# Optimization experiments

Measured on AMD Instinct MI355X. Metric: run time of the kernel, lower is better.

The kernel has to match this reference:

```python
import jax, jax.numpy as jnp
import numpy as np

B, L, D = 16, 1024, 256  # batch, c_len == q_len (required by the expand/add in the source), 2*d_model


def mask_logits(x, m):
    # Faithful to the source's (unusual) masking: x*m + x*(1-m)*1e30
    return x * m + x * (1.0 - m) * 1e30


def setup_inputs() -> dict:
    key = jax.random.key(0)
    k = jax.random.split(key, 7)
    c = jax.random.normal(k[0], (B, L, D), dtype=jnp.float32)
    q = jax.random.normal(k[1], (B, L, D), dtype=jnp.float32)
    c_mask = jnp.ones((B, 1, L), dtype=jnp.float32)
    q_mask = jnp.ones((B, 1, L), dtype=jnp.float32)
    # Learned parameters (nn.Parameter zeros in the source; random here so the test is non-degenerate)
    c_weight = jax.random.normal(k[2], (D, 1), dtype=jnp.float32) * 0.05
    q_weight = jax.random.normal(k[3], (D, 1), dtype=jnp.float32) * 0.05
    cq_weight = jax.random.normal(k[4], (1, 1, D), dtype=jnp.float32) * 0.05
    bias = jnp.zeros((1,), dtype=jnp.float32)
    return {"c": c, "q": q, "c_mask": c_mask, "q_mask": q_mask,
            "c_weight": c_weight, "q_weight": q_weight,
            "cq_weight": cq_weight, "bias": bias}


def reference(c, q, c_mask, q_mask, c_weight, q_weight, cq_weight, bias):
    # Dropout treated as identity (inference) for a deterministic reference.
    s0 = jnp.matmul(c, c_weight)                      # [B, L, 1] -> broadcasts over q_len
    s1 = jnp.swapaxes(jnp.matmul(c, q_weight), 1, 2)  # [B, 1, L] (source uses c here, not q)
    s2 = jnp.einsum('bid,bjd->bij', c * cq_weight, q) # [B, L, L]
    S = s0 + s1 + s2 + bias                           # trilinear similarity
    S1 = jax.nn.softmax(mask_logits(S, q_mask), axis=-1)              # [B, Lc, Lq]
    C2Q = jnp.matmul(S1, q)                                           # [B, Lc, D]
    # torch F.softmax with no dim on a 3D tensor defaults to dim=0 (legacy behavior) -> axis=0
    S2 = jax.nn.softmax(mask_logits(jnp.swapaxes(S, 1, 2), c_mask), axis=0)  # [B, Lq, Lc]
    S2 = jnp.matmul(S1, S2)                                           # [B, Lc, Lc]
    Q2C = jnp.matmul(S2, c)                                           # [B, Lc, D]
    # torch.cat default dim=0 -> [4B, Lc, D]
    return jnp.concatenate((c, C2Q, c * C2Q, c * Q2C), axis=0)
```

## Files before the change

kernel.cpp:

```cpp
#include <hip/hip_runtime.h>

typedef __bf16 bf16;
typedef _Float16 f16;
typedef __attribute__((ext_vector_type(8))) __bf16 bf16x8;
typedef __attribute__((ext_vector_type(4))) __bf16 bf16x4;
typedef __attribute__((ext_vector_type(8))) _Float16 f16x8;
typedef __attribute__((ext_vector_type(4))) _Float16 f16x4;
typedef __attribute__((ext_vector_type(4))) float f32x4;

constexpr int Bn = 16, Ln = 1024, Dn = 256;

__device__ __forceinline__ float maskf(float m) { return m + (1.0f - m) * 1e30f; }

__device__ __forceinline__ void gload16(const void* g, void* l) {
  __builtin_amdgcn_global_load_lds((const __attribute__((address_space(1))) void*)g,
                                   (__attribute__((address_space(3))) void*)l, 16, 0, 0);
}

#define VMCNT(N) asm volatile("s_waitcnt vmcnt(" #N ")" ::: "memory")
#define LGKM0 asm volatile("s_waitcnt lgkmcnt(0)" ::: "memory")
#define BARR                                  \
  do {                                        \
    asm volatile("" ::: "memory");            \
    __builtin_amdgcn_s_barrier();             \
    asm volatile("" ::: "memory");            \
  } while (0)

__device__ __forceinline__ void stageB128(const bf16* __restrict__ B, int ldb, int k0,
                                          bf16* lB, int tid, int wid) {
#pragma unroll
  for (int p = 0; p < 2; ++p) {
    int c0 = tid + (p << 8);
    int row = c0 >> 2, kk = (c0 & 3) << 3;
    gload16(B + (size_t)row * ldb + k0 + kk, lB + ((p << 8) + (wid << 6)) * 8);
  }
}

__device__ __forceinline__ void stage512(const bf16* __restrict__ G, int ldg, int k0,
                                         bf16* L, int tid, int wid) {
#pragma unroll
  for (int p = 0; p < 2; ++p) {
    int u = tid + (p << 9);
    int row = u >> 3, s = u & 7;
    int kk = ((s ^ (row & 7)) << 3);
    gload16(G + (size_t)row * ldg + k0 + kk, L + ((p << 9) + (wid << 6)) * 8);
  }
}

__device__ __forceinline__ const bf16* swzp(const bf16* L, int row, int slot) {
  return L + row * 64 + ((slot ^ (row & 7)) << 3);
}

__global__ __launch_bounds__(256) void k_prep2(
    const float* __restrict__ c, const float* __restrict__ q,
    const float* __restrict__ cw, const float* __restrict__ qw,
    const float* __restrict__ cqw, bf16* __restrict__ cm, bf16* __restrict__ qb,
    bf16* __restrict__ cT, bf16* __restrict__ qT,
    float* __restrict__ s0, float* __restrict__ s1, float* __restrict__ outc) {
  __shared__ __align__(16) bf16 tc[32][264];
  __shared__ __align__(16) bf16 tq[32][264];
  int blk = blockIdx.x;
  int b = blk >> 5;
  int l0 = (blk & 31) << 5;
  int t = threadIdx.x;
  int rl = t >> 3;
  int c0 = (t & 7) << 5;
  int grow = b * Ln + l0 + rl;
  size_t base = (size_t)grow * Dn + c0;
  float4 cv[8], qv[8];
#pragma unroll
  for (int k = 0; k < 8; ++k) {
    cv[k] = *(const float4*)&c[base + k * 4];
    qv[k] = *(const float4*)&q[base + k * 4];
  }
  float d0 = 0.f, d1 = 0.f;
#pragma unroll
  for (int k = 0; k < 8; ++k) {
    float4 w = *(const float4*)&cw[c0 + k * 4];
    float4 u = *(const float4*)&qw[c0 + k * 4];
    d0 += cv[k].x * w.x + cv[k].y * w.y + cv[k].z * w.z + cv[k].w * w.w;
    d1 += cv[k].x * u.x + cv[k].y * u.y + cv[k].z * u.z + cv[k].w * u.w;
  }
  d0 += __shfl_xor(d0, 1); d0 += __shfl_xor(d0, 2); d0 += __shfl_xor(d0, 4);
  d1 += __shfl_xor(d1, 1); d1 += __shfl_xor(d1, 2); d1 += __shfl_xor(d1, 4);
  if ((t & 7) == 0) { s0[grow] = d0; s1[grow] = d1; }
#pragma unroll
  for (int k = 0; k < 8; ++k) *(float4*)&outc[base + k * 4] = cv[k];
#pragma unroll
  for (int k2 = 0; k2 < 4; ++k2) {
    float4 m0 = *(const float4*)&cqw[c0 + k2 * 8];
    float4 m1 = *(const float4*)&cqw[c0 + k2 * 8 + 4];
    bf16x8 vm, vq, vc;
#pragma unroll
    for (int e = 0; e < 8; ++e) {
      float cvv = ((const float*)&cv[k2 * 2 + (e >> 2)])[e & 3];
      float qvv = ((const float*)&qv[k2 * 2 + (e >> 2)])[e & 3];
      float mw = (e < 4) ? ((const float*)&m0)[e] : ((const float*)&m1)[e - 4];
      vm[e] = (bf16)(cvv * mw);
      vq[e] = (bf16)qvv;
      vc[e] = (bf16)cvv;
    }
    *(bf16x8*)&cm[base + k2 * 8] = vm;
    *(bf16x8*)&qb[base + k2 * 8] = vq;
    *(bf16x8*)&tc[rl][c0 + k2 * 8] = vc;
    *(bf16x8*)&tq[rl][c0 + k2 * 8] = vq;
  }
  __syncthreads();
  int d = t;
  size_t tb = ((size_t)b * Dn + d) * Ln + l0;
  bf16x8 o[4];
#pragma unroll
  for (int j = 0; j < 4; ++j)
#pragma unroll
    for (int e = 0; e < 8; ++e) o[j][e] = tc[j * 8 + e][d];
#pragma unroll
  for (int j = 0; j < 4; ++j) *(bf16x8*)&cT[tb + j * 8] = o[j];
#pragma unroll
  for (int j = 0; j < 4; ++j)
#pragma unroll
    for (int e = 0; e < 8; ++e) o[j][e] = tq[j * 8 + e][d];
#pragma unroll
  for (int j = 0; j < 4; ++j) *(bf16x8*)&qT[tb + j * 8] = o[j];
}

__global__ __launch_bounds__(256) void g_s(const bf16* __restrict__ Am,
                                           const bf16* __restrict__ Bm,
                                           const float* __restrict__ s0,
                                           const float* __restrict__ s1,
                                           const float* __restrict__ bias,
                                           f16* __restrict__ S) {
  __shared__ __align__(16) bf16 lds[2][256 * 32];
  int f = blockIdx.x;
  int o = (f & 7) * 128 + (f >> 3);
  int bx = o & 7, by = (o >> 3) & 7, b = o >> 6;
  const bf16* Ab = Am + (size_t)b * Ln * Dn + (size_t)by * 128 * Dn;
  const bf16* Bb = Bm + (size_t)b * Ln * Dn + (size_t)bx * 128 * Dn;
  const int tid = threadIdx.x, wid = tid >> 6, lane = tid & 63;
  const int r = lane & 15, h = lane >> 4, wr = wid >> 1, wc = wid & 1;
  f32x4 acc[4][4];
  f32x4 zero = {0.f, 0.f, 0.f, 0.f};
#pragma unroll
  for (int i = 0; i < 4; ++i)
#pragma unroll
    for (int j = 0; j < 4; ++j) acc[i][j] = zero;

  stageB128(Ab, Dn, 0, &lds[0][0], tid, wid);
  stageB128(Bb, Dn, 0, &lds[0][128 * 32], tid, wid);
  for (int t = 0; t < 8; ++t) {
    int cur = t & 1;
    if (t < 7) {
      stageB128(Ab, Dn, (t + 1) * 32, &lds[cur ^ 1][0], tid, wid);
      stageB128(Bb, Dn, (t + 1) * 32, &lds[cur ^ 1][128 * 32], tid, wid);
      VMCNT(4);
    } else {
      VMCNT(0);
    }
    BARR;
    const bf16* lA = &lds[cur][0];
    const bf16* lB = &lds[cur][128 * 32];
    bf16x8 av[4], bv[4];
#pragma unroll
    for (int i = 0; i < 4; ++i) {
      av[i] = *(const bf16x8*)(lA + ((wr << 6) + (i << 4) + r) * 32 + (h << 3));
      bv[i] = *(const bf16x8*)(lB + ((wc << 6) + (i << 4) + r) * 32 + (h << 3));
    }
#pragma unroll
    for (int i = 0; i < 4; ++i)
#pragma unroll
      for (int j = 0; j < 4; ++j)
        acc[i][j] = __builtin_amdgcn_mfma_f32_16x16x32_bf16(av[i], bv[j], acc[i][j], 0, 0, 0);
    LGKM0; BARR;
  }
  int grow = by * 128 + wr * 64, gcol = bx * 128 + wc * 64;
  float bvv = bias[0];
  size_t sb = (size_t)b * Ln * Ln;
#pragma unroll
  for (int j = 0; j < 4; ++j) {
    int n = gcol + j * 16 + r;
    float v1 = s1[b * Ln + n];
#pragma unroll
    for (int i = 0; i < 4; ++i) {
      int mb = grow + i * 16 + h * 4;
#pragma unroll
      for (int g = 0; g < 4; ++g) {
        float v0 = s0[b * Ln + mb + g];
        S[sb + (size_t)(mb + g) * Ln + n] = (f16)(acc[i][j][g] + v0 + v1 + bvv);
      }
    }
  }
}

__global__ __launch_bounds__(256) void k_rowsoftmax(const f16* __restrict__ S,
                                                    const float* __restrict__ qmask,
                                                    bf16* __restrict__ P1) {
  int t = threadIdx.x;
  int row = blockIdx.x * 4 + (t >> 6);
  int b = row >> 10;
  int lane = t & 63;
  const f16* Sr = S + (size_t)row * Ln;
  const float* qm = qmask + (size_t)b * Ln;
  float v[16];
  float mx = -3.4e38f;
#pragma unroll
  for (int p = 0; p < 2; ++p) {
    f16x8 x = ((const f16x8*)Sr)[lane + (p << 6)];
    float4 m0 = ((const float4*)qm)[(lane + (p << 6)) * 2];
    float4 m1 = ((const float4*)qm)[(lane + (p << 6)) * 2 + 1];
    float mm[8] = {m0.x, m0.y, m0.z, m0.w, m1.x, m1.y, m1.z, m1.w};
#pragma unroll
    for (int e = 0; e < 8; ++e) {
      float xv = (float)x[e] * maskf(mm[e]);
      v[8 * p + e] = xv;
      mx = fmaxf(mx, xv);
    }
  }
#pragma unroll
  for (int off = 32; off; off >>= 1) mx = fmaxf(mx, __shfl_xor(mx, off));
  float sum = 0.f;
#pragma unroll
  for (int k = 0; k < 16; ++k) {
    v[k] = __expf(v[k] - mx);
    sum += v[k];
  }
#pragma unroll
  for (int off = 32; off; off >>= 1) sum += __shfl_xor(sum, off);
  float inv = 1.0f / sum;
  bf16* Pr = P1 + (size_t)row * Ln;
#pragma unroll
  for (int p = 0; p < 2; ++p) {
    bf16x8 o;
#pragma unroll
    for (int e = 0; e < 8; ++e) o[e] = (bf16)(v[8 * p + e] * inv);
    ((bf16x8*)Pr)[lane + (p << 6)] = o;
  }
}

__global__ __launch_bounds__(256) void k_bp2(const f16* __restrict__ S,
                                             const float* __restrict__ cmask,
                                             bf16* __restrict__ P2) {
  __shared__ __align__(16) bf16 tile[16][32][36];
  int i0 = blockIdx.y * 32, j0 = blockIdx.x * 32;
  int t = threadIdx.x;
  int ti = t >> 3, tj4 = (t & 7) << 2;
  int i = i0 + ti;
  const f16* Sp = S + (size_t)i * Ln + j0 + tj4;
  float fm[16];
#pragma unroll
  for (int b = 0; b < 16; ++b) fm[b] = maskf(cmask[b * Ln + i]);
  f16x4 u[16];
#pragma unroll
  for (int b = 0; b < 16; ++b) u[b] = *(const f16x4*)(Sp + (size_t)b * Ln * Ln);
  float m[4] = {-3.4e38f, -3.4e38f, -3.4e38f, -3.4e38f};
#pragma unroll
  for (int b = 0; b < 16; ++b)
#pragma unroll
    for (int g = 0; g < 4; ++g) m[g] = fmaxf(m[g], (float)u[b][g] * fm[b]);
  float e[16][4];
  float s[4] = {0.f, 0.f, 0.f, 0.f};
#pragma unroll
  for (int b = 0; b < 16; ++b)
#pragma unroll
    for (int g = 0; g < 4; ++g) {
      e[b][g] = __expf((float)u[b][g] * fm[b] - m[g]);
      s[g] += e[b][g];
    }
#pragma unroll
  for (int g = 0; g < 4; ++g) s[g] = 1.0f / s[g];
#pragma unroll
  for (int b = 0; b < 16; ++b)
#pragma unroll
    for (int g = 0; g < 4; ++g) tile[b][tj4 + g][ti] = (bf16)(e[b][g] * s[g]);
  __syncthreads();
  int jl = t >> 3, i4 = (t & 7) << 2;
#pragma unroll
  for (int b = 0; b < 16; ++b) {
    *(bf16x4*)&P2[((size_t)b * Ln + j0 + jl) * Ln + i0 + i4] =
        *(const bf16x4*)&tile[b][jl][i4];
  }
}

__global__ __launch_bounds__(512) void g_t(const bf16* __restrict__ cT,
                                           const bf16* __restrict__ P2,
                                           bf16* __restrict__ TT) {
  __shared__ __align__(16) bf16 lds[2][2 * 128 * 64];
  int f = blockIdx.x;
  int o = (f & 7) * 32 + (f >> 3);
  int b = o >> 4, md = (o >> 3) & 1, nb = o & 7;
  const bf16* Ab = cT + (size_t)b * Dn * Ln + (size_t)md * 128 * Ln;
  const bf16* Bb = P2 + (size_t)b * Ln * Ln + (size_t)nb * 128 * Ln;
  const int tid = threadIdx.x, wid = tid >> 6, lane = tid & 63;
  const int r = lane & 15, h = lane >> 4, wr = wid >> 2, wc = wid & 3;
  f32x4 acc[4][2];
  f32x4 zero = {0.f, 0.f, 0.f, 0.f};
#pragma unroll
  for (int i = 0; i < 4; ++i)
#pragma unroll
    for (int j = 0; j < 2; ++j) acc[i][j] = zero;

  stage512(Ab, Ln, 0, &lds[0][0], tid, wid);
  stage512(Bb, Ln, 0, &lds[0][8192], tid, wid);
  for (int t = 0; t < 16; ++t) {
    int cur = t & 1;
    if (t < 15) {
      stage512(Ab, Ln, (t + 1) * 64, &lds[cur ^ 1][0], tid, wid);
      stage512(Bb, Ln, (t + 1) * 64, &lds[cur ^ 1][8192], tid, wid);
      VMCNT(4);
    } else {
      VMCNT(0);
    }
    BARR;
    const bf16* lA = &lds[cur][0];
    const bf16* lB = &lds[cur][8192];
#pragma unroll
    for (int kk2 = 0; kk2 < 2; ++kk2) {
      int slot = (kk2 << 2) | h;
      bf16x8 av[4], bv[2];
#pragma unroll
      for (int i = 0; i < 4; ++i)
        av[i] = *(const bf16x8*)swzp(lA, (wr << 6) + (i << 4) + r, slot);
#pragma unroll
      for (int j = 0; j < 2; ++j)
        bv[j] = *(const bf16x8*)swzp(lB, (wc << 5) + (j << 4) + r, slot);
#pragma unroll
      for (int i = 0; i < 4; ++i)
#pragma unroll
        for (int j = 0; j < 2; ++j)
          acc[i][j] = __builtin_amdgcn_mfma_f32_16x16x32_bf16(av[i], bv[j], acc[i][j], 0, 0, 0);
    }
    LGKM0; BARR;
  }
  size_t ob = (size_t)b * Dn * Ln;
  int dbase = md * 128 + wr * 64, cbase = nb * 128 + wc * 32;
#pragma unroll
  for (int i = 0; i < 4; ++i)
#pragma unroll
    for (int j = 0; j < 2; ++j) {
      int n = cbase + j * 16 + r;
#pragma unroll
      for (int g = 0; g < 4; ++g)
        TT[ob + (size_t)(dbase + i * 16 + h * 4 + g) * Ln + n] = (bf16)acc[i][j][g];
    }
}

__global__ __launch_bounds__(512) void g_cq(const bf16* __restrict__ P1,
                                            const bf16* __restrict__ qT,
                                            const bf16* __restrict__ TT,
                                            const float* __restrict__ c,
                                            float* __restrict__ out) {
  __shared__ __align__(16) bf16 lds[2][3 * 128 * 64];
  int f = blockIdx.x;
  int o = (f & 7) * 32 + (f >> 3);
  int b = o >> 4, by = (o >> 1) & 7, bx = o & 1;
  const bf16* Ab = P1 + (size_t)b * Ln * Ln + (size_t)by * 128 * Ln;
  const bf16* B1 = qT + (size_t)b * Dn * Ln + (size_t)bx * 128 * Ln;
  const bf16* B2 = TT + (size_t)b * Dn * Ln + (size_t)bx * 128 * Ln;
  const int tid = threadIdx.x, wid = tid >> 6, lane = tid & 63;
  const int r = lane & 15, h = lane >> 4, wr = wid >> 2, wc = wid & 3;
  f32x4 acc1[4][2], acc2[4][2];
  f32x4 zero = {0.f, 0.f, 0.f, 0.f};
#pragma unroll
  for (int i = 0; i < 4; ++i)
#pragma unroll
    for (int j = 0; j < 2; ++j) { acc1[i][j] = zero; acc2[i][j] = zero; }

  stage512(Ab, Ln, 0, &lds[0][0], tid, wid);
  stage512(B1, Ln, 0, &lds[0][8192], tid, wid);
  stage512(B2, Ln, 0, &lds[0][16384], tid, wid);
  for (int t = 0; t < 16; ++t) {
    int cur = t & 1;
    if (t < 15) {
      stage512(Ab, Ln, (t + 1) * 64, &lds[cur ^ 1][0], tid, wid);
      stage512(B1, Ln, (t + 1) * 64, &lds[cur ^ 1][8192], tid, wid);
      stage512(B2, Ln, (t + 1) * 64, &lds[cur ^ 1][16384], tid, wid);
      VMCNT(6);
    } else {
      VMCNT(0);
    }
    BARR;
    const bf16* lA = &lds[cur][0];
    const bf16* lB1 = &lds[cur][8192];
    const bf16* lB2 = &lds[cur][16384];
#pragma unroll
    for (int kk2 = 0; kk2 < 2; ++kk2) {
      int slot = (kk2 << 2) | h;
      bf16x8 av[4], bv[2];
#pragma unroll
      for (int i = 0; i < 4; ++i)
        av[i] = *(const bf16x8*)swzp(lA, (wr << 6) + (i << 4) + r, slot);
#pragma unroll
      for (int j = 0; j < 2; ++j)
        bv[j] = *(const bf16x8*)swzp(lB1, (wc << 5) + (j << 4) + r, slot);
#pragma unroll
      for (int i = 0; i < 4; ++i)
#pragma unroll
        for (int j = 0; j < 2; ++j)
          acc1[i][j] = __builtin_amdgcn_mfma_f32_16x16x32_bf16(av[i], bv[j], acc1[i][j], 0, 0, 0);
#pragma unroll
      for (int j = 0; j < 2; ++j)
        bv[j] = *(const bf16x8*)swzp(lB2, (wc << 5) + (j << 4) + r, slot);
#pragma unroll
      for (int i = 0; i < 4; ++i)
#pragma unroll
        for (int j = 0; j < 2; ++j)
          acc2[i][j] = __builtin_amdgcn_mfma_f32_16x16x32_bf16(av[i], bv[j], acc2[i][j], 0, 0, 0);
    }
    LGKM0; BARR;
  }

  int grow = by * 128 + wr * 64, gcol = bx * 128 + wc * 32;
  const float* cb = c + (size_t)b * Ln * Dn;
  float* o1 = out + (size_t)(1 * Bn + b) * Ln * Dn;
  float* o2 = out + (size_t)(2 * Bn + b) * Ln * Dn;
  float* o3 = out + (size_t)(3 * Bn + b) * Ln * Dn;
#pragma unroll
  for (int j = 0; j < 2; ++j) {
    int n = gcol + j * 16 + r;
#pragma unroll
    for (int i = 0; i < 4; ++i) {
      int mb = grow + i * 16 + h * 4;
#pragma unroll
      for (int g = 0; g < 4; ++g) {
        float v1 = acc1[i][j][g];
        float v2 = acc2[i][j][g];
        size_t off = (size_t)(mb + g) * Dn + n;
        float cc = cb[off];
        o1[off] = v1;
        o2[off] = cc * v1;
        o3[off] = cc * v2;
      }
    }
  }
}

extern "C" void kernel_launch(void* const* d_in, const int* in_sizes, int n_in,
                              void* d_out, int out_size, void* d_ws, size_t ws_size,
                              hipStream_t stream) {
  const float* c = (const float*)d_in[0];
  const float* q = (const float*)d_in[1];
  const float* cmask = (const float*)d_in[2];
  const float* qmask = (const float*)d_in[3];
  const float* cw = (const float*)d_in[4];
  const float* qw = (const float*)d_in[5];
  const float* cqw = (const float*)d_in[6];
  const float* bias = (const float*)d_in[7];
  float* out = (float*)d_out;

  char* w = (char*)d_ws;
  f16* S = (f16*)w;       w += (size_t)Bn * Ln * Ln * 2;
  bf16* P1 = (bf16*)w;    w += (size_t)Bn * Ln * Ln * 2;
  bf16* P2 = (bf16*)w;    w += (size_t)Bn * Ln * Ln * 2;
  bf16* cm = (bf16*)w;    w += (size_t)Bn * Ln * Dn * 2;
  bf16* qb = (bf16*)w;    w += (size_t)Bn * Ln * Dn * 2;
  bf16* cT = (bf16*)w;    w += (size_t)Bn * Dn * Ln * 2;
  bf16* qT = (bf16*)w;    w += (size_t)Bn * Dn * Ln * 2;
  bf16* TT = (bf16*)w;    w += (size_t)Bn * Dn * Ln * 2;
  float* s0 = (float*)w;  w += (size_t)Bn * Ln * 4;
  float* s1 = (float*)w;  w += (size_t)Bn * Ln * 4;
  if ((size_t)(w - (char*)d_ws) > ws_size) return;

  k_prep2<<<dim3(Bn * Ln / 32), 256, 0, stream>>>(c, q, cw, qw, cqw, cm, qb, cT, qT, s0, s1, out);
  g_s<<<dim3(1024), 256, 0, stream>>>(cm, qb, s0, s1, bias, S);
  k_rowsoftmax<<<dim3(Bn * Ln / 4), 256, 0, stream>>>(S, qmask, P1);
  k_bp2<<<dim3(Ln / 32, Ln / 32), 256, 0, stream>>>(S, cmask, P2);
  g_t<<<dim3(256), 512, 0, stream>>>(cT, P2, TT);
  g_cq<<<dim3(256), 512, 0, stream>>>(P1, qT, TT, c, out);
}
```

Measured before the change: 117.6 us.

## Retile S GEMM to 512 threads with swizzled K64 stages; merge softmax kernels

```diff
diff --git a/kernel.cpp b/kernel.cpp
--- a/kernel.cpp
+++ b/kernel.cpp
@@ -25,16 +25,6 @@
     __builtin_amdgcn_s_barrier();             \
     asm volatile("" ::: "memory");            \
   } while (0)
-
-__device__ __forceinline__ void stageB128(const bf16* __restrict__ B, int ldb, int k0,
-                                          bf16* lB, int tid, int wid) {
-#pragma unroll
-  for (int p = 0; p < 2; ++p) {
-    int c0 = tid + (p << 8);
-    int row = c0 >> 2, kk = (c0 & 3) << 3;
-    gload16(B + (size_t)row * ldb + k0 + kk, lB + ((p << 8) + (wid << 6)) * 8);
-  }
-}
 
 __device__ __forceinline__ void stage512(const bf16* __restrict__ G, int ldg, int k0,
                                          bf16* L, int tid, int wid) {
@@ -123,59 +113,64 @@
   for (int j = 0; j < 4; ++j) *(bf16x8*)&qT[tb + j * 8] = o[j];
 }
 
-__global__ __launch_bounds__(256) void g_s(const bf16* __restrict__ Am,
+__global__ __launch_bounds__(512) void g_s(const bf16* __restrict__ Am,
                                            const bf16* __restrict__ Bm,
                                            const float* __restrict__ s0,
                                            const float* __restrict__ s1,
                                            const float* __restrict__ bias,
                                            f16* __restrict__ S) {
-  __shared__ __align__(16) bf16 lds[2][256 * 32];
+  __shared__ __align__(16) bf16 lds[2][2 * 128 * 64];
   int f = blockIdx.x;
   int o = (f & 7) * 128 + (f >> 3);
   int bx = o & 7, by = (o >> 3) & 7, b = o >> 6;
   const bf16* Ab = Am + (size_t)b * Ln * Dn + (size_t)by * 128 * Dn;
   const bf16* Bb = Bm + (size_t)b * Ln * Dn + (size_t)bx * 128 * Dn;
   const int tid = threadIdx.x, wid = tid >> 6, lane = tid & 63;
-  const int r = lane & 15, h = lane >> 4, wr = wid >> 1, wc = wid & 1;
-  f32x4 acc[4][4];
+  const int r = lane & 15, h = lane >> 4, wr = wid >> 2, wc = wid & 3;
+  f32x4 acc[4][2];
   f32x4 zero = {0.f, 0.f, 0.f, 0.f};
 #pragma unroll
   for (int i = 0; i < 4; ++i)
 #pragma unroll
-    for (int j = 0; j < 4; ++j) acc[i][j] = zero;
-
-  stageB128(Ab, Dn, 0, &lds[0][0], tid, wid);
-  stageB128(Bb, Dn, 0, &lds[0][128 * 32], tid, wid);
-  for (int t = 0; t < 8; ++t) {
+    for (int j = 0; j < 2; ++j) acc[i][j] = zero;
+
+  stage512(Ab, Dn, 0, &lds[0][0], tid, wid);
+  stage512(Bb, Dn, 0, &lds[0][8192], tid, wid);
+  for (int t = 0; t < 4; ++t) {
     int cur = t & 1;
-    if (t < 7) {
-      stageB128(Ab, Dn, (t + 1) * 32, &lds[cur ^ 1][0], tid, wid);
-      stageB128(Bb, Dn, (t + 1) * 32, &lds[cur ^ 1][128 * 32], tid, wid);
+    if (t < 3) {
+      stage512(Ab, Dn, (t + 1) * 64, &lds[cur ^ 1][0], tid, wid);
+      stage512(Bb, Dn, (t + 1) * 64, &lds[cur ^ 1][8192], tid, wid);
       VMCNT(4);
     } else {
       VMCNT(0);
     }
     BARR;
     const bf16* lA = &lds[cur][0];
-    const bf16* lB = &lds[cur][128 * 32];
-    bf16x8 av[4], bv[4];
-#pragma unroll
-    for (int i = 0; i < 4; ++i) {
-      av[i] = *(const bf16x8*)(lA + ((wr << 6) + (i << 4) + r) * 32 + (h << 3));
-      bv[i] = *(const bf16x8*)(lB + ((wc << 6) + (i << 4) + r) * 32 + (h << 3));
-    }
-#pragma unroll
-    for (int i = 0; i < 4; ++i)
-#pragma unroll
-      for (int j = 0; j < 4; ++j)
-        acc[i][j] = __builtin_amdgcn_mfma_f32_16x16x32_bf16(av[i], bv[j], acc[i][j], 0, 0, 0);
+    const bf16* lB = &lds[cur][8192];
+#pragma unroll
+    for (int kk2 = 0; kk2 < 2; ++kk2) {
+      int slot = (kk2 << 2) | h;
+      bf16x8 av[4], bv[2];
+#pragma unroll
+      for (int i = 0; i < 4; ++i)
+        av[i] = *(const bf16x8*)swzp(lA, (wr << 6) + (i << 4) + r, slot);
+#pragma unroll
+      for (int j = 0; j < 2; ++j)
+        bv[j] = *(const bf16x8*)swzp(lB, (wc << 5) + (j << 4) + r, slot);
+#pragma unroll
+      for (int i = 0; i < 4; ++i)
+#pragma unroll
+        for (int j = 0; j < 2; ++j)
+          acc[i][j] = __builtin_amdgcn_mfma_f32_16x16x32_bf16(av[i], bv[j], acc[i][j], 0, 0, 0);
+    }
     LGKM0; BARR;
   }
-  int grow = by * 128 + wr * 64, gcol = bx * 128 + wc * 64;
+  int grow = by * 128 + wr * 64, gcol = bx * 128 + wc * 32;
   float bvv = bias[0];
   size_t sb = (size_t)b * Ln * Ln;
 #pragma unroll
-  for (int j = 0; j < 4; ++j) {
+  for (int j = 0; j < 2; ++j) {
     int n = gcol + j * 16 + r;
     float v1 = s1[b * Ln + n];
 #pragma unroll
@@ -190,92 +185,92 @@
   }
 }
 
-__global__ __launch_bounds__(256) void k_rowsoftmax(const f16* __restrict__ S,
-                                                    const float* __restrict__ qmask,
-                                                    bf16* __restrict__ P1) {
+__global__ __launch_bounds__(256) void k_sm(const f16* __restrict__ S,
+                                            const float* __restrict__ qmask,
+                                            const float* __restrict__ cmask,
+                                            bf16* __restrict__ P1,
+                                            bf16* __restrict__ P2) {
+  __shared__ __align__(16) bf16 tile[16][32][36];
+  int blk = blockIdx.x;
   int t = threadIdx.x;
-  int row = blockIdx.x * 4 + (t >> 6);
-  int b = row >> 10;
-  int lane = t & 63;
-  const f16* Sr = S + (size_t)row * Ln;
-  const float* qm = qmask + (size_t)b * Ln;
-  float v[16];
-  float mx = -3.4e38f;
-#pragma unroll
-  for (int p = 0; p < 2; ++p) {
-    f16x8 x = ((const f16x8*)Sr)[lane + (p << 6)];
-    float4 m0 = ((const float4*)qm)[(lane + (p << 6)) * 2];
-    float4 m1 = ((const float4*)qm)[(lane + (p << 6)) * 2 + 1];
-    float mm[8] = {m0.x, m0.y, m0.z, m0.w, m1.x, m1.y, m1.z, m1.w};
-#pragma unroll
-    for (int e = 0; e < 8; ++e) {
-      float xv = (float)x[e] * maskf(mm[e]);
-      v[8 * p + e] = xv;
-      mx = fmaxf(mx, xv);
-    }
-  }
-#pragma unroll
-  for (int off = 32; off; off >>= 1) mx = fmaxf(mx, __shfl_xor(mx, off));
-  float sum = 0.f;
-#pragma unroll
-  for (int k = 0; k < 16; ++k) {
-    v[k] = __expf(v[k] - mx);
-    sum += v[k];
-  }
-#pragma unroll
-  for (int off = 32; off; off >>= 1) sum += __shfl_xor(sum, off);
-  float inv = 1.0f / sum;
-  bf16* Pr = P1 + (size_t)row * Ln;
-#pragma unroll
-  for (int p = 0; p < 2; ++p) {
-    bf16x8 o;
-#pragma unroll
-    for (int e = 0; e < 8; ++e) o[e] = (bf16)(v[8 * p + e] * inv);
-    ((bf16x8*)Pr)[lane + (p << 6)] = o;
-  }
-}
-
-__global__ __launch_bounds__(256) void k_bp2(const f16* __restrict__ S,
-                                             const float* __restrict__ cmask,
-                                             bf16* __restrict__ P2) {
-  __shared__ __align__(16) bf16 tile[16][32][36];
-  int i0 = blockIdx.y * 32, j0 = blockIdx.x * 32;
-  int t = threadIdx.x;
-  int ti = t >> 3, tj4 = (t & 7) << 2;
-  int i = i0 + ti;
-  const f16* Sp = S + (size_t)i * Ln + j0 + tj4;
-  float fm[16];
-#pragma unroll
-  for (int b = 0; b < 16; ++b) fm[b] = maskf(cmask[b * Ln + i]);
-  f16x4 u[16];
-#pragma unroll
-  for (int b = 0; b < 16; ++b) u[b] = *(const f16x4*)(Sp + (size_t)b * Ln * Ln);
-  float m[4] = {-3.4e38f, -3.4e38f, -3.4e38f, -3.4e38f};
-#pragma unroll
-  for (int b = 0; b < 16; ++b)
-#pragma unroll
-    for (int g = 0; g < 4; ++g) m[g] = fmaxf(m[g], (float)u[b][g] * fm[b]);
-  float e[16][4];
-  float s[4] = {0.f, 0.f, 0.f, 0.f};
-#pragma unroll
-  for (int b = 0; b < 16; ++b)
-#pragma unroll
-    for (int g = 0; g < 4; ++g) {
-      e[b][g] = __expf((float)u[b][g] * fm[b] - m[g]);
-      s[g] += e[b][g];
-    }
-#pragma unroll
-  for (int g = 0; g < 4; ++g) s[g] = 1.0f / s[g];
-#pragma unroll
-  for (int b = 0; b < 16; ++b)
-#pragma unroll
-    for (int g = 0; g < 4; ++g) tile[b][tj4 + g][ti] = (bf16)(e[b][g] * s[g]);
-  __syncthreads();
-  int jl = t >> 3, i4 = (t & 7) << 2;
-#pragma unroll
-  for (int b = 0; b < 16; ++b) {
-    *(bf16x4*)&P2[((size_t)b * Ln + j0 + jl) * Ln + i0 + i4] =
-        *(const bf16x4*)&tile[b][jl][i4];
+  if (blk < 1024) {
+    int i0 = (blk >> 5) << 5, j0 = (blk & 31) << 5;
+    int ti = t >> 3, tj4 = (t & 7) << 2;
+    int i = i0 + ti;
+    const f16* Sp = S + (size_t)i * Ln + j0 + tj4;
+    float fm[16];
+#pragma unroll
+    for (int b = 0; b < 16; ++b) fm[b] = maskf(cmask[b * Ln + i]);
+    f16x4 u[16];
+#pragma unroll
+    for (int b = 0; b < 16; ++b) u[b] = *(const f16x4*)(Sp + (size_t)b * Ln * Ln);
+    float m[4] = {-3.4e38f, -3.4e38f, -3.4e38f, -3.4e38f};
+#pragma unroll
+    for (int b = 0; b < 16; ++b)
+#pragma unroll
+      for (int g = 0; g < 4; ++g) m[g] = fmaxf(m[g], (float)u[b][g] * fm[b]);
+    float e[16][4];
+    float s[4] = {0.f, 0.f, 0.f, 0.f};
+#pragma unroll
+    for (int b = 0; b < 16; ++b)
+#pragma unroll
+      for (int g = 0; g < 4; ++g) {
+        e[b][g] = __expf((float)u[b][g] * fm[b] - m[g]);
+        s[g] += e[b][g];
+      }
+#pragma unroll
+    for (int g = 0; g < 4; ++g) s[g] = 1.0f / s[g];
+#pragma unroll
+    for (int b = 0; b < 16; ++b)
+#pragma unroll
+      for (int g = 0; g < 4; ++g) tile[b][tj4 + g][ti] = (bf16)(e[b][g] * s[g]);
+    __syncthreads();
+    int jl = t >> 3, i4 = (t & 7) << 2;
+#pragma unroll
+    for (int b = 0; b < 16; ++b) {
+      *(bf16x4*)&P2[((size_t)b * Ln + j0 + jl) * Ln + i0 + i4] =
+          *(const bf16x4*)&tile[b][jl][i4];
+    }
+  } else {
+    int row = (blk - 1024) * 4 + (t >> 6);
+    int b = row >> 10;
+    int lane = t & 63;
+    const f16* Sr = S + (size_t)row * Ln;
+    const float* qm = qmask + (size_t)b * Ln;
+    float v[16];
+    float mx = -3.4e38f;
+#pragma unroll
+    for (int p = 0; p < 2; ++p) {
+      f16x8 x = ((const f16x8*)Sr)[lane + (p << 6)];
+      float4 m0 = ((const float4*)qm)[(lane + (p << 6)) * 2];
+      float4 m1 = ((const float4*)qm)[(lane + (p << 6)) * 2 + 1];
+      float mm[8] = {m0.x, m0.y, m0.z, m0.w, m1.x, m1.y, m1.z, m1.w};
+#pragma unroll
+      for (int e = 0; e < 8; ++e) {
+        float xv = (float)x[e] * maskf(mm[e]);
+        v[8 * p + e] = xv;
+        mx = fmaxf(mx, xv);
+      }
+    }
+#pragma unroll
+    for (int off = 32; off; off >>= 1) mx = fmaxf(mx, __shfl_xor(mx, off));
+    float sum = 0.f;
+#pragma unroll
+    for (int k = 0; k < 16; ++k) {
+      v[k] = __expf(v[k] - mx);
+      sum += v[k];
+    }
+#pragma unroll
+    for (int off = 32; off; off >>= 1) sum += __shfl_xor(sum, off);
+    float inv = 1.0f / sum;
+    bf16* Pr = P1 + (size_t)row * Ln;
+#pragma unroll
+    for (int p = 0; p < 2; ++p) {
+      bf16x8 o;
+#pragma unroll
+      for (int e = 0; e < 8; ++e) o[e] = (bf16)(v[8 * p + e] * inv);
+      ((bf16x8*)Pr)[lane + (p << 6)] = o;
+    }
   }
 }
 
@@ -459,9 +454,8 @@
   if ((size_t)(w - (char*)d_ws) > ws_size) return;
 
   k_prep2<<<dim3(Bn * Ln / 32), 256, 0, stream>>>(c, q, cw, qw, cqw, cm, qb, cT, qT, s0, s1, out);
-  g_s<<<dim3(1024), 256, 0, stream>>>(cm, qb, s0, s1, bias, S);
-  k_rowsoftmax<<<dim3(Bn * Ln / 4), 256, 0, stream>>>(S, qmask, P1);
-  k_bp2<<<dim3(Ln / 32, Ln / 32), 256, 0, stream>>>(S, cmask, P2);
+  g_s<<<dim3(1024), 512, 0, stream>>>(cm, qb, s0, s1, bias, S);
+  k_sm<<<dim3(1024 + Bn * Ln / 4), 256, 0, stream>>>(S, qmask, cmask, P1, P2);
   g_t<<<dim3(256), 512, 0, stream>>>(cT, P2, TT);
   g_cq<<<dim3(256), 512, 0, stream>>>(P1, qT, TT, c, out);
 }
```

Result: faster. 114.9 us (median of 2 runs) (-2.3%).
